# Kernel optimization log

Measured on AMD Instinct MI355X. Metric: run time of the kernel, lower is better.

Reference implementation:

```python
import jax, jax.numpy as jnp
import numpy as np

VOCAB = 30522
HIDDEN = 768
MAX_POS = 512
N_TYPES = 8
N_HEADS = 4
NHID = 128
LN_EPS = 1e-12
ALPHA = 0.01  # LeakyReLU slope
NEG = -9e15


def setup_inputs() -> dict:
    key = jax.random.key(0)
    ks = jax.random.split(key, 12)
    B, N = 8, 256
    token_ids = jax.random.randint(ks[0], (B, N), 0, VOCAB)
    type_ids = jax.random.randint(ks[1], (B, N), 0, 7)
    synset_ids = jax.random.randint(ks[2], (B, N), 0, 32)
    highway = jax.random.randint(ks[3], (B, N), 0, 2).astype(bool)
    tok_emb = jax.random.normal(ks[4], (VOCAB, HIDDEN), jnp.float32) * 0.02
    type_emb = jax.random.normal(ks[5], (N_TYPES, HIDDEN), jnp.float32) * 0.02
    pos_emb = jax.random.normal(ks[6], (MAX_POS, HIDDEN), jnp.float32) * 0.02
    ln_g = jnp.ones((HIDDEN,), jnp.float32)
    ln_b = jnp.zeros((HIDDEN,), jnp.float32)
    # GAT per-head params, xavier-ish scale
    W = jax.random.normal(ks[7], (N_HEADS, HIDDEN, NHID), jnp.float32) * (1.414 * (2.0 / (HIDDEN + NHID)) ** 0.5)
    a = jax.random.normal(ks[8], (N_HEADS, 2 * NHID), jnp.float32) * (1.414 * (2.0 / (2 * NHID + 1)) ** 0.5)
    out_W = jax.random.normal(ks[9], (VOCAB, N_HEADS * NHID), jnp.float32) * 0.02
    out_b = jnp.zeros((VOCAB,), jnp.float32)
    return {"token_ids": token_ids, "type_ids": type_ids, "synset_ids": synset_ids,
            "highway": highway, "tok_emb": tok_emb, "type_emb": type_emb,
            "pos_emb": pos_emb, "ln_g": ln_g, "ln_b": ln_b, "W": W, "a": a,
            "out_W": out_W, "out_b": out_b}


def _graph_mask(token_ids, type_ids, synset_ids, highway):
    # visibility: same synset, plus directed highway edges by type
    vis = synset_ids[:, :, None] == synset_ids[:, None, :]
    t, hw = type_ids, highway
    s1 = (t == 1) & hw
    s3 = (t == 3) & hw
    d1 = (jnp.isin(t, jnp.array([0, 2, 5]))) & hw
    d3 = (jnp.isin(t, jnp.array([6, 4, 0]))) & hw
    vis = vis | (s1[:, :, None] & d1[:, None, :]) | (s3[:, :, None] & d3[:, None, :])
    not_pad = token_ids != 0  # bert padding_idx == 0
    return vis & not_pad[:, None, :]  # (B,N,N)


def reference(token_ids, type_ids, synset_ids, highway, tok_emb, type_emb,
              pos_emb, ln_g, ln_b, W, a, out_W, out_b):
    B, N = token_ids.shape
    mask = _graph_mask(token_ids, type_ids, synset_ids, highway)
    # TaxoEmbedding (eval mode: no dropout)
    x = tok_emb[token_ids] + type_emb[type_ids] + pos_emb[:N][None]
    mu = jnp.mean(x, axis=-1, keepdims=True)
    var = jnp.mean((x - mu) ** 2, axis=-1, keepdims=True)
    x = (x - mu) * jax.lax.rsqrt(var + LN_EPS) * ln_g + ln_b
    # GAT heads. e[h,b,i,j] = leakyrelu(a1_h . Wh[b,i] + a2_h . Wh[b,j])
    Wh = jnp.einsum('bnd,hdf->hbnf', x, W)  # (H,B,N,F)
    F_ = W.shape[-1]
    a1, a2 = a[:, :F_], a[:, F_:]
    e = (jnp.einsum('hbnf,hf->hbn', Wh, a1)[:, :, :, None]
         + jnp.einsum('hbnf,hf->hbn', Wh, a2)[:, :, None, :])
    e = jnp.where(e > 0, e, ALPHA * e)
    e = jnp.where(mask[None], e, NEG)
    att = jax.nn.softmax(e, axis=2)  # torch softmax(dim=1) on (B,N,N) -> i axis
    hp = jax.nn.elu(jnp.einsum('hbij,hbjf->hbif', att, Wh))  # (H,B,N,F)
    cat = hp.transpose(1, 2, 0, 3).reshape(B, N, -1)  # head-major concat
    out = jax.nn.elu(cat @ out_W.T + out_b)
    return jax.nn.log_softmax(out, axis=-1)
```

## Files before the change

kernel.cpp:

```cpp
#include <hip/hip_runtime.h>
#include <hip/hip_bf16.h>

#define VOCAB 30522
#define VPAD 30592
#define HIDDEN 768
#define NHEADS 4
#define NHID 128
#define ROWS 2048
#define KDIM 512
#define LN_EPS 1e-12f
#define ALPHA_LR 0.01f
#define NEGV -9.0e15f
#define NTILE 239

typedef __attribute__((ext_vector_type(8))) short short8;
typedef __attribute__((ext_vector_type(4))) float floatx4;
typedef __attribute__((ext_vector_type(2))) float floatx2;
typedef __attribute__((ext_vector_type(4))) unsigned short ushort4v;
typedef __attribute__((ext_vector_type(8))) unsigned short ushort8v;

static __device__ __forceinline__ unsigned short f2bf(float f) {
  unsigned int u = __float_as_uint(f);
  unsigned int r = u + 0x7fffu + ((u >> 16) & 1u);
  return (unsigned short)(r >> 16);
}

static __device__ __forceinline__ void gload16(const unsigned short* g, unsigned short* l) {
  __builtin_amdgcn_global_load_lds(
      (const __attribute__((address_space(1))) void*)g,
      (__attribute__((address_space(3))) void*)l, 16, 0, 0);
}

__global__ __launch_bounds__(256) void k_prep(const float* __restrict__ out_W,
    unsigned short* __restrict__ owb,
    const float* __restrict__ W, unsigned short* __restrict__ Wt,
    const int* __restrict__ tok, const int* __restrict__ typ,
    const float* __restrict__ tok_emb, const float* __restrict__ type_emb, const float* __restrict__ pos_emb,
    const float* __restrict__ ln_g, const float* __restrict__ ln_b, unsigned short* __restrict__ xout) {
  __shared__ unsigned short T[128][136];
  __shared__ float red[8];
  int bid = blockIdx.x;
  if (bid < 2048) {
    int n4src = (VOCAB * KDIM) / 4, n4tot = (VPAD * KDIM) / 4;
    int i = bid * 256 + threadIdx.x;
    int stride = 2048 * 256;
    for (; i < n4tot; i += stride) {
      ushort4v o = {0, 0, 0, 0};
      if (i < n4src) {
        floatx4 v = reinterpret_cast<const floatx4*>(out_W)[i];
        o.x = f2bf(v.x); o.y = f2bf(v.y); o.z = f2bf(v.z); o.w = f2bf(v.w);
      }
      reinterpret_cast<ushort4v*>(owb)[i] = o;
    }
  } else if (bid < 2072) {
    int b = bid - 2048;
    int h = b & 3, dc = b >> 2;
    int tid = threadIdx.x;
    const float* Wb = W + ((long)h * HIDDEN + dc * 128) * NHID;
    #pragma unroll
    for (int q = 0; q < 16; q++) {
      int idx = q * 256 + tid;
      int d = idx >> 5, f4 = idx & 31;
      floatx4 v = *reinterpret_cast<const floatx4*>(&Wb[(long)d * NHID + f4 * 4]);
      #pragma unroll
      for (int j = 0; j < 4; j++) T[f4 * 4 + j][d] = f2bf(v[j]);
    }
    __syncthreads();
    int f = tid >> 1, rh = tid & 1;
    unsigned short* dst = Wt + (long)(h * 128 + f) * HIDDEN + dc * 128 + rh * 64;
    #pragma unroll
    for (int i = 0; i < 8; i++)
      *reinterpret_cast<ushort8v*>(&dst[i * 8]) =
          *reinterpret_cast<const ushort8v*>(&T[f][rh * 64 + i * 8]);
  } else {
    int row = bid - 2072;
    int n = row & 255;
    int t = tok[row], ty = typ[row];
    const float* te = tok_emb + (long)t * HIDDEN;
    const float* ye = type_emb + (long)ty * HIDDEN;
    const float* pe = pos_emb + (long)n * HIDDEN;
    float v[3]; float s = 0.f, ss = 0.f;
    #pragma unroll
    for (int q = 0; q < 3; q++) {
      int d = threadIdx.x + q * 256;
      float x = te[d] + ye[d] + pe[d];
      v[q] = x; s += x; ss += x * x;
    }
    for (int off = 32; off; off >>= 1) { s += __shfl_down(s, off); ss += __shfl_down(ss, off); }
    int wid = threadIdx.x >> 6;
    if ((threadIdx.x & 63) == 0) { red[wid] = s; red[4 + wid] = ss; }
    __syncthreads();
    if (threadIdx.x == 0) {
      float a = red[0] + red[1] + red[2] + red[3];
      float b2 = red[4] + red[5] + red[6] + red[7];
      float mu = a * (1.0f / 768.0f);
      float var = b2 * (1.0f / 768.0f) - mu * mu;
      red[0] = mu; red[1] = rsqrtf(var + LN_EPS);
    }
    __syncthreads();
    float mu = red[0], rstd = red[1];
    #pragma unroll
    for (int q = 0; q < 3; q++) {
      int d = threadIdx.x + q * 256;
      xout[(long)row * HIDDEN + d] = f2bf((v[q] - mu) * rstd * ln_g[d] + ln_b[d]);
    }
  }
}

__global__ __launch_bounds__(256) void k_wh(const unsigned short* __restrict__ A,
    const unsigned short* __restrict__ Bw, float* __restrict__ Wh) {
  int mt = blockIdx.x & 15, nt = blockIdx.x >> 4;
  int m0 = mt * 128, n0 = nt * 128;
  __shared__ __align__(16) unsigned short Al[2][128 * 64];
  __shared__ __align__(16) unsigned short Bl[2][128 * 64];
  int tid = threadIdx.x;
  int l = tid & 63, wid = tid >> 6;
  int wr = wid >> 1, wc = wid & 1;
  int lrow = l & 15, lgrp = l >> 4;
  floatx4 acc[4][4];
  #pragma unroll
  for (int i = 0; i < 4; i++)
    #pragma unroll
    for (int j = 0; j < 4; j++) acc[i][j] = (floatx4){0.f, 0.f, 0.f, 0.f};
  const unsigned short* Ab = A + (long)m0 * HIDDEN;
  const unsigned short* Bb = Bw + (long)n0 * HIDDEN;

  auto STAGE = [&](int t, int bufi) {
    #pragma unroll
    for (int q = 0; q < 4; q++) {
      int chunk = q * 256 + tid;
      int row = chunk >> 3, kp = chunk & 7, swz = kp ^ (row & 7);
      long off = (long)row * HIDDEN + t * 64 + swz * 8;
      gload16(Ab + off, &Al[bufi][chunk * 8]);
      gload16(Bb + off, &Bl[bufi][chunk * 8]);
    }
  };

  STAGE(0, 0);
  STAGE(1, 1);
  asm volatile("s_waitcnt vmcnt(8)" ::: "memory");
  __builtin_amdgcn_sched_barrier(0);
  __builtin_amdgcn_s_barrier();

  #pragma unroll
  for (int kt = 0; kt < 12; kt++) {
    int cur = kt & 1;
    short8 af[2][4], bf[2][4];
    #pragma unroll
    for (int kk = 0; kk < 2; kk++) {
      int sA = (kk * 4 + lgrp) ^ (lrow & 7);
      #pragma unroll
      for (int mi = 0; mi < 4; mi++)
        af[kk][mi] = *reinterpret_cast<const short8*>(&Al[cur][(wr * 64 + mi * 16 + lrow) * 64 + sA * 8]);
      #pragma unroll
      for (int ni = 0; ni < 4; ni++)
        bf[kk][ni] = *reinterpret_cast<const short8*>(&Bl[cur][(wc * 64 + ni * 16 + lrow) * 64 + sA * 8]);
    }
    asm volatile("s_waitcnt lgkmcnt(0)" ::: "memory");
    __builtin_amdgcn_sched_barrier(0);
    __builtin_amdgcn_s_barrier();
    __builtin_amdgcn_sched_barrier(0);
    if (kt < 10) STAGE(kt + 2, cur);
    #pragma unroll
    for (int kk = 0; kk < 2; kk++)
      #pragma unroll
      for (int mi = 0; mi < 4; mi++)
        #pragma unroll
        for (int ni = 0; ni < 4; ni++)
          acc[mi][ni] = __builtin_amdgcn_mfma_f32_16x16x32_bf16(af[kk][mi], bf[kk][ni], acc[mi][ni], 0, 0, 0);
    if (kt < 10) {
      asm volatile("s_waitcnt vmcnt(8)" ::: "memory");
    } else if (kt == 10) {
      asm volatile("s_waitcnt vmcnt(0)" ::: "memory");
    }
    __builtin_amdgcn_sched_barrier(0);
    if (kt < 11) __builtin_amdgcn_s_barrier();
  }

  #pragma unroll
  for (int mi = 0; mi < 4; mi++) {
    #pragma unroll
    for (int reg = 0; reg < 4; reg++) {
      int row = m0 + wr * 64 + mi * 16 + lgrp * 4 + reg;
      #pragma unroll
      for (int ni = 0; ni < 4; ni++) {
        int c = n0 + wc * 64 + ni * 16 + lrow;
        int h = c >> 7, f = c & 127;
        Wh[((long)h * ROWS + row) * NHID + f] = acc[mi][ni][reg];
      }
    }
  }
}

__device__ __forceinline__ unsigned char mk_flags(int t, int hwv, int tokv) {
  unsigned char fl = 0;
  if (hwv) {
    if (t == 1) fl |= 1;
    if (t == 3) fl |= 2;
    if (t == 0 || t == 2 || t == 5) fl |= 4;
    if (t == 6 || t == 4 || t == 0) fl |= 8;
  }
  if (tokv != 0) fl |= 16;
  return fl;
}

__global__ __launch_bounds__(256) void k_ecol(const int* __restrict__ tok, const int* __restrict__ typ,
    const int* __restrict__ syn, const int* __restrict__ hw,
    const float* __restrict__ Wh, const float* __restrict__ a,
    float* __restrict__ e1, float* __restrict__ e2,
    float* __restrict__ colmax, float* __restrict__ colrs) {
  int h = blockIdx.x >> 3, b = blockIdx.x & 7;
  __shared__ float av[256];
  __shared__ float E1[256]; __shared__ int SY[256]; __shared__ unsigned char FL[256];
  int tid = threadIdx.x;
  int g = b * 256 + tid;
  av[tid] = a[h * 256 + tid];
  FL[tid] = mk_flags(typ[g], hw[g], tok[g]);
  SY[tid] = syn[g];
  __syncthreads();
  const float* wr = Wh + ((long)h * ROWS + g) * NHID;
  float s1 = 0.f, s2 = 0.f;
  #pragma unroll 8
  for (int f = 0; f < 128; f++) { float w = wr[f]; s1 += w * av[f]; s2 += w * av[128 + f]; }
  e1[h * ROWS + g] = s1; e2[h * ROWS + g] = s2;
  E1[tid] = s1;
  __syncthreads();
  float e2j = s2;
  int syj = SY[tid]; unsigned char flj = FL[tid];
  bool npj = flj & 16, d1j = flj & 4, d3j = flj & 8;
  float m = -INFINITY;
  for (int i = 0; i < 256; i++) {
    float e = E1[i] + e2j;
    e = e > 0.f ? e : ALPHA_LR * e;
    unsigned char fli = FL[i];
    bool vis = (SY[i] == syj) || ((fli & 1) && d1j) || ((fli & 2) && d3j);
    float v = (vis && npj) ? e : NEGV;
    m = fmaxf(m, v);
  }
  float s = 0.f;
  for (int i = 0; i < 256; i++) {
    float e = E1[i] + e2j;
    e = e > 0.f ? e : ALPHA_LR * e;
    unsigned char fli = FL[i];
    bool vis = (SY[i] == syj) || ((fli & 1) && d1j) || ((fli & 2) && d3j);
    float v = (vis && npj) ? e : NEGV;
    s += __expf(v - m);
  }
  int idx = (h * 8 + b) * 256 + tid;
  colmax[idx] = m;
  colrs[idx] = 1.0f / s;
}

__global__ __launch_bounds__(256) void k_att(const int* __restrict__ tok, const int* __restrict__ typ,
    const int* __restrict__ syn, const int* __restrict__ hw,
    const float* __restrict__ e1, const float* __restrict__ e2,
    const float* __restrict__ colmax, const float* __restrict__ colrs,
    const float* __restrict__ Wh, unsigned short* __restrict__ cat) {
  int chunk = blockIdx.x & 7; int hb = blockIdx.x >> 3;
  int h = hb >> 3, b = hb & 7;
  __shared__ float E2[256], CM[256], CR[256];
  __shared__ int SY[256]; __shared__ unsigned char FL[256];
  __shared__ float WJ[64][128];
  int tid = threadIdx.x;
  {
    int g = b * 256 + tid;
    FL[tid] = mk_flags(typ[g], hw[g], tok[g]);
    E2[tid] = e2[h * ROWS + g];
    CM[tid] = colmax[hb * 256 + tid];
    CR[tid] = colrs[hb * 256 + tid];
    SY[tid] = syn[g];
  }
  __syncthreads();
  int i = chunk * 32 + (tid >> 3);
  int gi = b * 256 + i;
  float e1i = e1[h * ROWS + gi];
  unsigned char fli = FL[i];
  bool s1i = fli & 1, s3i = fli & 2;
  int syni = SY[i];
  int f0 = tid & 7;
  floatx4 acc4[4];
  #pragma unroll
  for (int k2 = 0; k2 < 4; k2++) acc4[k2] = (floatx4){0.f, 0.f, 0.f, 0.f};
  for (int j0 = 0; j0 < 256; j0 += 64) {
    #pragma unroll
    for (int q = 0; q < 8; q++) {
      int e = tid + q * 256;
      int j = e >> 5, f4 = e & 31;
      *reinterpret_cast<floatx4*>(&WJ[j][f4 * 4]) =
          *reinterpret_cast<const floatx4*>(&Wh[((long)h * ROWS + b * 256 + j0 + j) * NHID + f4 * 4]);
    }
    __syncthreads();
    for (int j = 0; j < 64; j++) {
      int jj = j0 + j;
      unsigned char flj = FL[jj];
      bool vis = (syni == SY[jj]) || (s1i && (flj & 4)) || (s3i && (flj & 8));
      bool msk = vis && (flj & 16);
      float ev = e1i + E2[jj];
      ev = ev > 0.f ? ev : ALPHA_LR * ev;
      float v = msk ? ev : NEGV;
      float w = __expf(v - CM[jj]) * CR[jj];
      #pragma unroll
      for (int k2 = 0; k2 < 4; k2++) {
        floatx4 wv = *reinterpret_cast<const floatx4*>(&WJ[j][(f0 + 8 * k2) * 4]);
        acc4[k2] += wv * w;
      }
    }
    __syncthreads();
  }
  ushort4v* cr4 = reinterpret_cast<ushort4v*>(cat + (long)gi * KDIM + h * NHID);
  #pragma unroll
  for (int k2 = 0; k2 < 4; k2++) {
    ushort4v o4;
    #pragma unroll
    for (int e = 0; e < 4; e++) {
      float v = acc4[k2][e];
      v = v > 0.f ? v : __expf(v) - 1.f;
      o4[e] = f2bf(v);
    }
    cr4[f0 + 8 * k2] = o4;
  }
}

__global__ __launch_bounds__(256) void k_gemm(const unsigned short* __restrict__ A,
    const unsigned short* __restrict__ Bw, const float* __restrict__ bias,
    unsigned short* __restrict__ otmp) {
  int bid = blockIdx.x;
  bid = (bid & 7) * ((16 * NTILE) >> 3) + (bid >> 3);
  int mt = bid & 15, nt = bid >> 4;
  int m0 = mt * 128, n0 = nt * 128;
  __shared__ __align__(16) char smem[65536];
  unsigned short (*Al)[128 * 64] = reinterpret_cast<unsigned short (*)[128 * 64]>(smem);
  unsigned short (*Bl)[128 * 64] = reinterpret_cast<unsigned short (*)[128 * 64]>(smem + 32768);
  unsigned short* Cl = reinterpret_cast<unsigned short*>(smem);
  int tid = threadIdx.x;
  int l = tid & 63, wid = tid >> 6;
  int wr = wid >> 1, wc = wid & 1;
  int lrow = l & 15, lgrp = l >> 4;
  floatx4 acc[4][4];
  #pragma unroll
  for (int i = 0; i < 4; i++)
    #pragma unroll
    for (int j = 0; j < 4; j++) acc[i][j] = (floatx4){0.f, 0.f, 0.f, 0.f};
  const unsigned short* Ab = A + (long)m0 * KDIM;
  const unsigned short* Bb = Bw + (long)n0 * KDIM;

  auto STAGE = [&](int t, int bufi) {
    #pragma unroll
    for (int q = 0; q < 4; q++) {
      int chunk = q * 256 + tid;
      int row = chunk >> 3, kp = chunk & 7, swz = kp ^ (row & 7);
      long off = (long)row * KDIM + t * 64 + swz * 8;
      gload16(Ab + off, &Al[bufi][chunk * 8]);
      gload16(Bb + off, &Bl[bufi][chunk * 8]);
    }
  };

  STAGE(0, 0);
  STAGE(1, 1);
  asm volatile("s_waitcnt vmcnt(8)" ::: "memory");
  __builtin_amdgcn_sched_barrier(0);
  __builtin_amdgcn_s_barrier();

  #pragma unroll
  for (int kt = 0; kt < 8; kt++) {
    int cur = kt & 1;
    short8 af[2][4], bf[2][4];
    #pragma unroll
    for (int kk = 0; kk < 2; kk++) {
      int sA = (kk * 4 + lgrp) ^ (lrow & 7);
      #pragma unroll
      for (int mi = 0; mi < 4; mi++)
        af[kk][mi] = *reinterpret_cast<const short8*>(&Al[cur][(wr * 64 + mi * 16 + lrow) * 64 + sA * 8]);
      #pragma unroll
      for (int ni = 0; ni < 4; ni++)
        bf[kk][ni] = *reinterpret_cast<const short8*>(&Bl[cur][(wc * 64 + ni * 16 + lrow) * 64 + sA * 8]);
    }
    asm volatile("s_waitcnt lgkmcnt(0)" ::: "memory");
    __builtin_amdgcn_sched_barrier(0);
    __builtin_amdgcn_s_barrier();
    __builtin_amdgcn_sched_barrier(0);
    if (kt < 6) STAGE(kt + 2, cur);
    #pragma unroll
    for (int kk = 0; kk < 2; kk++)
      #pragma unroll
      for (int mi = 0; mi < 4; mi++)
        #pragma unroll
        for (int ni = 0; ni < 4; ni++)
          acc[mi][ni] = __builtin_amdgcn_mfma_f32_16x16x32_bf16(af[kk][mi], bf[kk][ni], acc[mi][ni], 0, 0, 0);
    if (kt < 6) {
      asm volatile("s_waitcnt vmcnt(8)" ::: "memory");
    } else if (kt == 6) {
      asm volatile("s_waitcnt vmcnt(0)" ::: "memory");
    }
    __builtin_amdgcn_sched_barrier(0);
    if (kt < 7) __builtin_amdgcn_s_barrier();
  }

  float bcol[4];
  #pragma unroll
  for (int ni = 0; ni < 4; ni++) {
    int c = n0 + wc * 64 + ni * 16 + lrow;
    bcol[ni] = (c < VOCAB) ? bias[c] : 0.f;
  }
  #pragma unroll
  for (int mi = 0; mi < 4; mi++)
    #pragma unroll
    for (int ni = 0; ni < 4; ni++)
      #pragma unroll
      for (int reg = 0; reg < 4; reg++) {
        int r = wr * 64 + mi * 16 + lgrp * 4 + reg;
        int c = wc * 64 + ni * 16 + lrow;
        float z = acc[mi][ni][reg] + bcol[ni];
        float o = z > 0.f ? z : __expf(z) - 1.f;
        Cl[r * 136 + c] = f2bf(o);
      }
  __syncthreads();
  #pragma unroll
  for (int it = 0; it < 8; it++) {
    int r = it * 16 + (tid >> 4);
    int c = (tid & 15) * 8;
    int gc = n0 + c;
    ushort8v v = *reinterpret_cast<const ushort8v*>(&Cl[r * 136 + c]);
    unsigned short* orow = otmp + (long)(m0 + r) * 2 * VOCAB;
    if (gc + 8 <= VOCAB) {
      *reinterpret_cast<ushort8v*>(orow + gc) = v;
    } else {
      #pragma unroll
      for (int e = 0; e < 8; e++)
        if (gc + e < VOCAB) orow[gc + e] = v[e];
    }
  }
}

__global__ __launch_bounds__(1024) void k_sub(float* __restrict__ out) {
  int row = blockIdx.x;
  float* rb = out + (long)row * VOCAB;
  const unsigned int* src = reinterpret_cast<const unsigned int*>(rb);
  int tid = threadIdx.x;
  unsigned int v[15];
  float se = 0.f;
  #pragma unroll
  for (int i = 0; i < 15; i++) {
    int p = tid + i * 1024;
    v[i] = (p < VOCAB / 2) ? src[p] : 0u;
  }
  #pragma unroll
  for (int i = 0; i < 15; i++) {
    int p = tid + i * 1024;
    if (p < VOCAB / 2) {
      unsigned int u = v[i];
      float lo = __uint_as_float((u & 0xffffu) << 16);
      float hi = __uint_as_float(u & 0xffff0000u);
      se += __expf(lo) + __expf(hi);
    }
  }
  #pragma unroll
  for (int off = 32; off; off >>= 1) se += __shfl_xor(se, off);
  __shared__ float red[16];
  int wid = tid >> 6;
  if ((tid & 63) == 0) red[wid] = se;
  __syncthreads();
  if (tid < 16) {
    float r = red[tid];
    #pragma unroll
    for (int off = 8; off; off >>= 1) r += __shfl_xor(r, off);
    if (tid == 0) red[0] = logf(r);
  }
  __syncthreads();
  float L = red[0];
  floatx2* dst = reinterpret_cast<floatx2*>(rb);
  #pragma unroll
  for (int i = 0; i < 15; i++) {
    int p = tid + i * 1024;
    if (p < VOCAB / 2) {
      unsigned int u = v[i];
      float lo = __uint_as_float((u & 0xffffu) << 16);
      float hi = __uint_as_float(u & 0xffff0000u);
      floatx2 o; o.x = lo - L; o.y = hi - L;
      dst[p] = o;
    }
  }
}

extern "C" void kernel_launch(void* const* d_in, const int* in_sizes, int n_in,
                              void* d_out, int out_size, void* d_ws, size_t ws_size,
                              hipStream_t stream) {
  const int* tok = (const int*)d_in[0];
  const int* typ = (const int*)d_in[1];
  const int* syn = (const int*)d_in[2];
  const int* hw  = (const int*)d_in[3];
  const float* tok_emb  = (const float*)d_in[4];
  const float* type_emb = (const float*)d_in[5];
  const float* pos_emb  = (const float*)d_in[6];
  const float* ln_g = (const float*)d_in[7];
  const float* ln_b = (const float*)d_in[8];
  const float* W    = (const float*)d_in[9];
  const float* a    = (const float*)d_in[10];
  const float* out_W = (const float*)d_in[11];
  const float* out_b = (const float*)d_in[12];
  float* out = (float*)d_out;
  char* ws = (char*)d_ws;
  unsigned short* xb = (unsigned short*)(ws + 0);
  float* Wh  = (float*)(ws + 3145728);
  float* e1  = (float*)(ws + 7340032);
  float* e2  = (float*)(ws + 7372800);
  float* cm  = (float*)(ws + 7405568);
  float* cs  = (float*)(ws + 7438336);
  unsigned short* cat = (unsigned short*)(ws + 7471104);
  unsigned short* Wt  = (unsigned short*)(ws + 9568256);
  unsigned short* owb = (unsigned short*)(ws + 10354688);

  k_prep<<<4120, 256, 0, stream>>>(out_W, owb, W, Wt, tok, typ,
                                   tok_emb, type_emb, pos_emb, ln_g, ln_b, xb);
  k_wh<<<64, 256, 0, stream>>>(xb, Wt, Wh);
  k_ecol<<<32, 256, 0, stream>>>(tok, typ, syn, hw, Wh, a, e1, e2, cm, cs);
  k_att<<<256, 256, 0, stream>>>(tok, typ, syn, hw, e1, e2, cm, cs, Wh, cat);
  k_gemm<<<16 * NTILE, 256, 0, stream>>>(cat, owb, out_b, (unsigned short*)out);
  k_sub<<<2048, 1024, 0, stream>>>(out);
}
```

Before: 302.7 us.

## Enlarge output GEMM tiles to 256x256 with 512 threads and interleaved fragment loads

Grows the vocab-projection GEMM tile from 128x128 to 256x256, using 8 waves per block that each own a 128x64 sub-tile. The vocab padding is widened to match. Within each k-step, LDS fragment loads are interleaved with MFMA groups in a ping-pong order so reads overlap compute. The aim is more data reuse per global load and fewer blocks. The cost is 128KB of LDS per block, which limits occupancy. The unpadded 256-wide epilogue staging buffer may also hit LDS bank conflicts.

```diff
diff --git a/kernel.cpp b/kernel.cpp
--- a/kernel.cpp
+++ b/kernel.cpp
@@ -2,7 +2,7 @@
 #include <hip/hip_bf16.h>
 
 #define VOCAB 30522
-#define VPAD 30592
+#define VPAD 30720
 #define HIDDEN 768
 #define NHEADS 4
 #define NHID 128
@@ -11,7 +11,7 @@
 #define LN_EPS 1e-12f
 #define ALPHA_LR 0.01f
 #define NEGV -9.0e15f
-#define NTILE 239
+#define NT256 120
 
 typedef __attribute__((ext_vector_type(8))) short short8;
 typedef __attribute__((ext_vector_type(4))) float floatx4;
@@ -321,24 +321,24 @@
   }
 }
 
-__global__ __launch_bounds__(256) void k_gemm(const unsigned short* __restrict__ A,
+__global__ __launch_bounds__(512, 2) void k_gemm(const unsigned short* __restrict__ A,
     const unsigned short* __restrict__ Bw, const float* __restrict__ bias,
     unsigned short* __restrict__ otmp) {
   int bid = blockIdx.x;
-  bid = (bid & 7) * ((16 * NTILE) >> 3) + (bid >> 3);
-  int mt = bid & 15, nt = bid >> 4;
-  int m0 = mt * 128, n0 = nt * 128;
-  __shared__ __align__(16) char smem[65536];
-  unsigned short (*Al)[128 * 64] = reinterpret_cast<unsigned short (*)[128 * 64]>(smem);
-  unsigned short (*Bl)[128 * 64] = reinterpret_cast<unsigned short (*)[128 * 64]>(smem + 32768);
+  int lin = (bid & 7) * NT256 + (bid >> 3);
+  int mt = lin & 7, nt = lin >> 3;
+  int m0 = mt * 256, n0 = nt * 256;
+  __shared__ __align__(16) char smem[131072];
+  unsigned short (*Al)[256 * 64] = reinterpret_cast<unsigned short (*)[256 * 64]>(smem);
+  unsigned short (*Bl)[256 * 64] = reinterpret_cast<unsigned short (*)[256 * 64]>(smem + 65536);
   unsigned short* Cl = reinterpret_cast<unsigned short*>(smem);
   int tid = threadIdx.x;
   int l = tid & 63, wid = tid >> 6;
-  int wr = wid >> 1, wc = wid & 1;
+  int wr = wid >> 2, wc = wid & 3;
   int lrow = l & 15, lgrp = l >> 4;
-  floatx4 acc[4][4];
-  #pragma unroll
-  for (int i = 0; i < 4; i++)
+  floatx4 acc[8][4];
+  #pragma unroll
+  for (int i = 0; i < 8; i++)
     #pragma unroll
     for (int j = 0; j < 4; j++) acc[i][j] = (floatx4){0.f, 0.f, 0.f, 0.f};
   const unsigned short* Ab = A + (long)m0 * KDIM;
@@ -347,7 +347,7 @@
   auto STAGE = [&](int t, int bufi) {
     #pragma unroll
     for (int q = 0; q < 4; q++) {
-      int chunk = q * 256 + tid;
+      int chunk = q * 512 + tid;
       int row = chunk >> 3, kp = chunk & 7, swz = kp ^ (row & 7);
       long off = (long)row * KDIM + t * 64 + swz * 8;
       gload16(Ab + off, &Al[bufi][chunk * 8]);
@@ -364,29 +364,74 @@
   #pragma unroll
   for (int kt = 0; kt < 8; kt++) {
     int cur = kt & 1;
-    short8 af[2][4], bf[2][4];
-    #pragma unroll
-    for (int kk = 0; kk < 2; kk++) {
-      int sA = (kk * 4 + lgrp) ^ (lrow & 7);
-      #pragma unroll
-      for (int mi = 0; mi < 4; mi++)
-        af[kk][mi] = *reinterpret_cast<const short8*>(&Al[cur][(wr * 64 + mi * 16 + lrow) * 64 + sA * 8]);
-      #pragma unroll
-      for (int ni = 0; ni < 4; ni++)
-        bf[kk][ni] = *reinterpret_cast<const short8*>(&Bl[cur][(wc * 64 + ni * 16 + lrow) * 64 + sA * 8]);
-    }
-    asm volatile("s_waitcnt lgkmcnt(0)" ::: "memory");
-    __builtin_amdgcn_sched_barrier(0);
-    __builtin_amdgcn_s_barrier();
-    __builtin_amdgcn_sched_barrier(0);
-    if (kt < 6) STAGE(kt + 2, cur);
-    #pragma unroll
-    for (int kk = 0; kk < 2; kk++)
+    short8 afr[8];
+    short8 bfr[4];
+    #pragma unroll
+    for (int mi = 0; mi < 4; mi++)
+      #pragma unroll
+      for (int ks = 0; ks < 2; ks++)
+        afr[mi * 2 + ks] = *reinterpret_cast<const short8*>(
+            &Al[cur][(wr * 128 + mi * 16 + lrow) * 64 + (((ks * 4 + lgrp) ^ (lrow & 7)) * 8)]);
+    #pragma unroll
+    for (int ni = 0; ni < 2; ni++)
+      #pragma unroll
+      for (int ks = 0; ks < 2; ks++)
+        bfr[ni * 2 + ks] = *reinterpret_cast<const short8*>(
+            &Bl[cur][(wc * 64 + ni * 16 + lrow) * 64 + (((ks * 4 + lgrp) ^ (lrow & 7)) * 8)]);
+    #pragma unroll
+    for (int ks = 0; ks < 2; ks++)
       #pragma unroll
       for (int mi = 0; mi < 4; mi++)
         #pragma unroll
-        for (int ni = 0; ni < 4; ni++)
-          acc[mi][ni] = __builtin_amdgcn_mfma_f32_16x16x32_bf16(af[kk][mi], bf[kk][ni], acc[mi][ni], 0, 0, 0);
+        for (int ni = 0; ni < 2; ni++)
+          acc[mi][ni] = __builtin_amdgcn_mfma_f32_16x16x32_bf16(afr[mi * 2 + ks], bfr[ni * 2 + ks], acc[mi][ni], 0, 0, 0);
+    __builtin_amdgcn_sched_barrier(0);
+    #pragma unroll
+    for (int ni = 0; ni < 2; ni++)
+      #pragma unroll
+      for (int ks = 0; ks < 2; ks++)
+        bfr[ni * 2 + ks] = *reinterpret_cast<const short8*>(
+            &Bl[cur][(wc * 64 + (2 + ni) * 16 + lrow) * 64 + (((ks * 4 + lgrp) ^ (lrow & 7)) * 8)]);
+    #pragma unroll
+    for (int ks = 0; ks < 2; ks++)
+      #pragma unroll
+      for (int mi = 0; mi < 4; mi++)
+        #pragma unroll
+        for (int ni = 0; ni < 2; ni++)
+          acc[mi][2 + ni] = __builtin_amdgcn_mfma_f32_16x16x32_bf16(afr[mi * 2 + ks], bfr[ni * 2 + ks], acc[mi][2 + ni], 0, 0, 0);
+    __builtin_amdgcn_sched_barrier(0);
+    #pragma unroll
+    for (int mi = 0; mi < 4; mi++)
+      #pragma unroll
+      for (int ks = 0; ks < 2; ks++)
+        afr[mi * 2 + ks] = *reinterpret_cast<const short8*>(
+            &Al[cur][(wr * 128 + (4 + mi) * 16 + lrow) * 64 + (((ks * 4 + lgrp) ^ (lrow & 7)) * 8)]);
+    #pragma unroll
+    for (int ks = 0; ks < 2; ks++)
+      #pragma unroll
+      for (int mi = 0; mi < 4; mi++)
+        #pragma unroll
+        for (int ni = 0; ni < 2; ni++)
+          acc[4 + mi][2 + ni] = __builtin_amdgcn_mfma_f32_16x16x32_bf16(afr[mi * 2 + ks], bfr[ni * 2 + ks], acc[4 + mi][2 + ni], 0, 0, 0);
+    __builtin_amdgcn_sched_barrier(0);
+    #pragma unroll
+    for (int ni = 0; ni < 2; ni++)
+      #pragma unroll
+      for (int ks = 0; ks < 2; ks++)
+        bfr[ni * 2 + ks] = *reinterpret_cast<const short8*>(
+            &Bl[cur][(wc * 64 + ni * 16 + lrow) * 64 + (((ks * 4 + lgrp) ^ (lrow & 7)) * 8)]);
+    asm volatile("s_waitcnt lgkmcnt(0)" ::: "memory");
+    __builtin_amdgcn_sched_barrier(0);
+    __builtin_amdgcn_s_barrier();
+    __builtin_amdgcn_sched_barrier(0);
+    if (kt < 6) STAGE(kt + 2, cur);
+    #pragma unroll
+    for (int ks = 0; ks < 2; ks++)
+      #pragma unroll
+      for (int mi = 0; mi < 4; mi++)
+        #pragma unroll
+        for (int ni = 0; ni < 2; ni++)
+          acc[4 + mi][ni] = __builtin_amdgcn_mfma_f32_16x16x32_bf16(afr[mi * 2 + ks], bfr[ni * 2 + ks], acc[4 + mi][ni], 0, 0, 0);
     if (kt < 6) {
       asm volatile("s_waitcnt vmcnt(8)" ::: "memory");
     } else if (kt == 6) {
@@ -395,7 +440,6 @@
     __builtin_amdgcn_sched_barrier(0);
     if (kt < 7) __builtin_amdgcn_s_barrier();
   }
-
   float bcol[4];
   #pragma unroll
   for (int ni = 0; ni < 4; ni++) {
@@ -403,24 +447,24 @@
     bcol[ni] = (c < VOCAB) ? bias[c] : 0.f;
   }
   #pragma unroll
-  for (int mi = 0; mi < 4; mi++)
+  for (int mi = 0; mi < 8; mi++)
     #pragma unroll
     for (int ni = 0; ni < 4; ni++)
       #pragma unroll
       for (int reg = 0; reg < 4; reg++) {
-        int r = wr * 64 + mi * 16 + lgrp * 4 + reg;
+        int r = wr * 128 + mi * 16 + lgrp * 4 + reg;
         int c = wc * 64 + ni * 16 + lrow;
         float z = acc[mi][ni][reg] + bcol[ni];
         float o = z > 0.f ? z : __expf(z) - 1.f;
-        Cl[r * 136 + c] = f2bf(o);
+        Cl[r * 256 + c] = f2bf(o);
       }
   __syncthreads();
   #pragma unroll
-  for (int it = 0; it < 8; it++) {
-    int r = it * 16 + (tid >> 4);
-    int c = (tid & 15) * 8;
-    int gc = n0 + c;
-    ushort8v v = *reinterpret_cast<const ushort8v*>(&Cl[r * 136 + c]);
+  for (int it = 0; it < 16; it++) {
+    int idx = it * 512 + tid;
+    int r = idx >> 5, c8 = (idx & 31) * 8;
+    int gc = n0 + c8;
+    ushort8v v = *reinterpret_cast<const ushort8v*>(&Cl[r * 256 + c8]);
     unsigned short* orow = otmp + (long)(m0 + r) * 2 * VOCAB;
     if (gc + 8 <= VOCAB) {
       *reinterpret_cast<ushort8v*>(orow + gc) = v;
@@ -515,6 +559,6 @@
   k_wh<<<64, 256, 0, stream>>>(xb, Wt, Wh);
   k_ecol<<<32, 256, 0, stream>>>(tok, typ, syn, hw, Wh, a, e1, e2, cm, cs);
   k_att<<<256, 256, 0, stream>>>(tok, typ, syn, hw, e1, e2, cm, cs, Wh, cat);
-  k_gemm<<<16 * NTILE, 256, 0, stream>>>(cat, owb, out_b, (unsigned short*)out);
+  k_gemm<<<8 * NT256, 512, 0, stream>>>(cat, owb, out_b, (unsigned short*)out);
   k_sub<<<2048, 1024, 0, stream>>>(out);
 }
```

Measured after the change: 301.8 us. No clear change (-0.3%).
